# Optimization experiments

Measured on AMD Instinct MI355X. Metric: run time of the kernel, lower is better.

Reference implementation:

```python
import jax, jax.numpy as jnp
import numpy as np

N_NODES = 50_000
N_EDGES = 1_600_000
N_VMS = 10_000
N_SCORE = 1_000_000
D_IN, D_E, D_OUT = 128, 64, 64
MLP_IN, MLP_H, MLP_OUT = 64, 128, 64
H1, H2 = 50, 25  # GNNTower fixed hidden widths


def setup_inputs() -> dict:
    key = jax.random.key(0)
    ks = jax.random.split(key, 24)
    w = lambda k, s: (jax.random.normal(k, s, jnp.float32) * 0.05)
    return {
        "component_features": jax.random.normal(ks[0], (N_NODES, D_IN), jnp.float32),
        "component_edges_features": jax.random.normal(ks[1], (N_EDGES, D_E), jnp.float32),
        "vm_features": jax.random.normal(ks[2], (N_VMS, MLP_IN), jnp.float32),
        "src": jax.random.randint(ks[3], (N_EDGES,), 0, N_NODES, jnp.int32),
        "dst": jax.random.randint(ks[4], (N_EDGES,), 0, N_NODES, jnp.int32),
        "e_comp": jax.random.randint(ks[5], (N_SCORE,), 0, N_NODES, jnp.int32),
        "e_vm": jax.random.randint(ks[6], (N_SCORE,), 0, N_VMS, jnp.int32),
        # GNN layer 1: W_msg [D_IN+D_E, H1], W_apply [D_IN+H1, H1]
        "Wm1": w(ks[7], (D_IN + D_E, H1)), "bm1": jnp.zeros((H1,), jnp.float32),
        "Wa1": w(ks[8], (D_IN + H1, H1)), "ba1": jnp.zeros((H1,), jnp.float32),
        # GNN layer 2
        "Wm2": w(ks[9], (H1 + D_E, H2)), "bm2": jnp.zeros((H2,), jnp.float32),
        "Wa2": w(ks[10], (H1 + H2, H2)), "ba2": jnp.zeros((H2,), jnp.float32),
        # GNN layer 3
        "Wm3": w(ks[11], (H2 + D_E, D_OUT)), "bm3": jnp.zeros((D_OUT,), jnp.float32),
        "Wa3": w(ks[12], (H2 + D_OUT, D_OUT)), "ba3": jnp.zeros((D_OUT,), jnp.float32),
        # MLP tower
        "Wmlp1": w(ks[13], (MLP_IN, MLP_H)), "bmlp1": jnp.zeros((MLP_H,), jnp.float32),
        "Wmlp2": w(ks[14], (MLP_H, MLP_OUT)), "bmlp2": jnp.zeros((MLP_OUT,), jnp.float32),
    }


def reference(component_features, component_edges_features, vm_features,
              src, dst, e_comp, e_vm,
              Wm1, bm1, Wa1, ba1, Wm2, bm2, Wa2, ba2, Wm3, bm3, Wa3, ba3,
              Wmlp1, bmlp1, Wmlp2, bmlp2):
    ef = component_edges_features

    def gnn_layer(h, Wm, bm, Wa, ba):
        d = h.shape[-1]
        # message: relu(W_msg @ concat(h[src], efeat)) == gather + split matmul (avoids concat copy)
        m = jax.nn.relu(h[src] @ Wm[:d] + ef @ Wm[d:] + bm)  # [E, out]
        # scatter-sum aggregation into destination nodes
        h_neigh = jax.ops.segment_sum(m, dst, num_segments=N_NODES)  # [N, out]
        # apply: relu(W_apply @ concat(h, h_neigh))
        return jax.nn.relu(h @ Wa[:d] + h_neigh @ Wa[d:] + ba)

    h = gnn_layer(component_features, Wm1, bm1, Wa1, ba1)   # [N, 50]
    h = gnn_layer(h, Wm2, bm2, Wa2, ba2)                    # [N, 25]  (dropout = identity in eval)
    h = gnn_layer(h, Wm3, bm3, Wa3, ba3)                    # [N, D_OUT]

    vm = jax.nn.relu(vm_features @ Wmlp1 + bmlp1) @ Wmlp2 + bmlp2  # [V, MLP_OUT]

    # sum over concat(comp_emb[e_comp], vm_emb[e_vm]) == sum of parts
    scores = jnp.sum(h, axis=-1)[e_comp] + jnp.sum(vm, axis=-1)[e_vm]  # [N_SCORE]
    return jax.nn.sigmoid(scores)
```

## Files before the change

### kernel.cpp

```cpp
#include <hip/hip_runtime.h>

typedef unsigned int uint;
typedef unsigned short ushort;
typedef short bf16x8 __attribute__((ext_vector_type(8)));
typedef float f32x4  __attribute__((ext_vector_type(4)));


__device__ __forceinline__ ushort f2bf(float f) {
    uint u = __float_as_uint(f);
    u += 0x7FFFu + ((u >> 16) & 1u);
    return (ushort)(u >> 16);
}
__device__ __forceinline__ float bf2f(uint s) {
    return __uint_as_float(s << 16);
}

template<int K0, int KP0, int K1, int KP1, int KC, int OUT, int WOUT,
         int NTC, int RPT, int MODE>
__global__ __launch_bounds__(256) void tile_gemm(
    const float* __restrict__ X0, int sx0,
    const float* __restrict__ X1, int sx1,
    const float* __restrict__ Wg, const float* __restrict__ Bg,
    float* __restrict__ Y, int sy, int nR)
{
    constexpr int KPT  = KP0 + KP1;
    constexpr int C4   = KC / 4;
    constexpr int OUTP = 4 * NTC;
    constexpr int NTR  = 256 / NTC;
    constexpr int TR   = NTR * RPT;
    static_assert(TR == 128, "tile must be 128 rows");
    static_assert(KPT % KC == 0, "KC must divide KPT");

    __shared__ float4 Xl[TR * C4];
    __shared__ float4 Wl[KC * NTC];
    __shared__ float  __align__(16) bl[OUTP];

    const int tid = threadIdx.x;
    const int r0  = blockIdx.x * TR;

    for (int idx = tid; idx < OUTP; idx += 256)
        bl[idx] = (Bg != nullptr && idx < OUT) ? Bg[idx] : 0.f;

    const int tc  = tid & (NTC - 1);
    const int tr  = tid / NTC;
    const int key = (RPT * tr) >> 3;

    float4 acc[RPT];
    #pragma unroll
    for (int i = 0; i < RPT; i++) acc[i] = make_float4(0.f, 0.f, 0.f, 0.f);

    for (int kc0 = 0; kc0 < KPT; kc0 += KC) {
        if (kc0 != 0) __syncthreads();
        for (int idx = tid; idx < TR * C4; idx += 256) {
            int r = idx / C4, c = idx - r * C4;
            int col = kc0 + 4 * c;
            int gr = r0 + r;
            float4 v = make_float4(0.f, 0.f, 0.f, 0.f);
            if (gr < nR) {
                if (KP1 == 0 || col < KP0)
                    v = *reinterpret_cast<const float4*>(X0 + (long long)gr * sx0 + col);
                else
                    v = *reinterpret_cast<const float4*>(X1 + (long long)gr * sx1 + (col - KP0));
            }
            int cs = c + ((r >> 3) % C4); if (cs >= C4) cs -= C4;
            Xl[r * C4 + cs] = v;
        }
        for (int idx = tid; idx < KC * OUTP; idx += 256) {
            int kl = idx / OUTP, o = idx - kl * OUTP;
            int k = kc0 + kl;
            float v = 0.f;
            if (o < OUT) {
                if (k < KP0) { if (k < K0) v = Wg[k * OUT + o]; }
                else { int kk = k - KP0; if (kk < K1) v = Wg[(K0 + kk) * OUT + o]; }
            }
            ((float*)Wl)[kl * OUTP + o] = v;
        }
        __syncthreads();

        const int km = key % C4;
        #pragma unroll 4
        for (int k4 = 0; k4 < C4; k4++) {
            int cs = k4 + km; if (cs >= C4) cs -= C4;
            float4 x[RPT];
            #pragma unroll
            for (int i = 0; i < RPT; i++)
                x[i] = Xl[(RPT * tr + i) * C4 + cs];
            #pragma unroll
            for (int kk = 0; kk < 4; kk++) {
                float4 w = Wl[(4 * k4 + kk) * NTC + tc];
                #pragma unroll
                for (int i = 0; i < RPT; i++) {
                    float xs = (kk == 0) ? x[i].x : (kk == 1) ? x[i].y
                             : (kk == 2) ? x[i].z : x[i].w;
                    acc[i].x = fmaf(xs, w.x, acc[i].x);
                    acc[i].y = fmaf(xs, w.y, acc[i].y);
                    acc[i].z = fmaf(xs, w.z, acc[i].z);
                    acc[i].w = fmaf(xs, w.w, acc[i].w);
                }
            }
        }
    }

    const float4 b4 = reinterpret_cast<float4*>(bl)[tc];
    const int o = 4 * tc;

    if (MODE == 0 || MODE == 1) {
        if (o < WOUT) {
            #pragma unroll
            for (int i = 0; i < RPT; i++) {
                int gr = r0 + RPT * tr + i;
                if (gr < nR) {
                    float4 v;
                    v.x = acc[i].x + b4.x; v.y = acc[i].y + b4.y;
                    v.z = acc[i].z + b4.z; v.w = acc[i].w + b4.w;
                    if (MODE == 1) {
                        v.x = fmaxf(v.x, 0.f); v.y = fmaxf(v.y, 0.f);
                        v.z = fmaxf(v.z, 0.f); v.w = fmaxf(v.w, 0.f);
                    }
                    *reinterpret_cast<float4*>(Y + (long long)gr * sy + o) = v;
                }
            }
        }
    } else {
        #pragma unroll
        for (int i = 0; i < RPT; i++) {
            int gr = r0 + RPT * tr + i;
            float s = fmaxf(acc[i].x + b4.x, 0.f) + fmaxf(acc[i].y + b4.y, 0.f)
                    + fmaxf(acc[i].z + b4.z, 0.f) + fmaxf(acc[i].w + b4.w, 0.f);
            #pragma unroll
            for (int off = 1; off < NTC; off <<= 1) s += __shfl_xor(s, off);
            if (tc == 0 && gr < nR) Y[gr] = s;
        }
    }
}

__global__ __launch_bounds__(256) void proj_all(
    const float* __restrict__ ef,
    const float* __restrict__ W1e, const float* __restrict__ W2e,
    const float* __restrict__ W3e, const int* __restrict__ invperm,
    ushort* __restrict__ G1, ushort* __restrict__ G2, ushort* __restrict__ G3,
    int nE)
{
    constexpr int NT  = 10;
    constexpr int CLP = 168;

    __shared__ ushort Al[64 * 64];
    __shared__ ushort Bl[NT * 128 * 8];
    __shared__ ushort Cl[64 * CLP];
    __shared__ int    sl_pos[64];

    const int tid = threadIdx.x;

    for (int idx = tid; idx < NT * 128; idx += 256) {
        int t  = idx >> 7;
        int ks = (idx >> 6) & 1;
        int l  = idx & 63;
        int gp  = t * 16 + (l & 15);
        int kb  = ks * 32 + ((l >> 4) << 3);
        ushort u[8];
        #pragma unroll
        for (int j = 0; j < 8; j++) {
            int k = kb + j;
            float w = 0.f;
            if (gp < 64)      { if (gp < 50) w = W1e[k * 50 + gp]; }
            else if (gp < 96) { int c = gp - 64; if (c < 25) w = W2e[k * 25 + c]; }
            else              { int c = gp - 96; w = W3e[k * 64 + c]; }
            u[j] = f2bf(w);
        }
        *reinterpret_cast<bf16x8*>(&Bl[idx * 8]) = *reinterpret_cast<bf16x8*>(u);
    }

    const int wv = tid >> 6;
    const int l  = tid & 63;
    const int ntiles = (nE + 63) >> 6;

    for (int tile = blockIdx.x; tile < ntiles; tile += gridDim.x) {
        const int r0 = tile << 6;
        __syncthreads();

        if (tid < 64) sl_pos[tid] = (r0 + tid < nE) ? invperm[r0 + tid] : -1;
        {
            int row = tid >> 2;
            int kq  = (tid & 3) << 4;
            int gr  = r0 + row;
            float4 f0 = {0,0,0,0}, f1 = {0,0,0,0}, f2 = {0,0,0,0}, f3 = {0,0,0,0};
            if (gr < nE) {
                const float* p = ef + (size_t)gr * 64 + kq;
                f0 = *reinterpret_cast<const float4*>(p);
                f1 = *reinterpret_cast<const float4*>(p + 4);
                f2 = *reinterpret_cast<const float4*>(p + 8);
                f3 = *reinterpret_cast<const float4*>(p + 12);
            }
            ushort u[16];
            u[0]=f2bf(f0.x); u[1]=f2bf(f0.y); u[2]=f2bf(f0.z); u[3]=f2bf(f0.w);
            u[4]=f2bf(f1.x); u[5]=f2bf(f1.y); u[6]=f2bf(f1.z); u[7]=f2bf(f1.w);
            u[8]=f2bf(f2.x); u[9]=f2bf(f2.y); u[10]=f2bf(f2.z); u[11]=f2bf(f2.w);
            u[12]=f2bf(f3.x); u[13]=f2bf(f3.y); u[14]=f2bf(f3.z); u[15]=f2bf(f3.w);
            int kc0 = ((kq >> 3) + 0) ^ (row & 7);
            int kc1 = ((kq >> 3) + 1) ^ (row & 7);
            *reinterpret_cast<bf16x8*>(&Al[(row << 6) + kc0 * 8]) = *reinterpret_cast<bf16x8*>(u);
            *reinterpret_cast<bf16x8*>(&Al[(row << 6) + kc1 * 8]) = *reinterpret_cast<bf16x8*>(u + 8);
        }
        __syncthreads();

        f32x4 acc[NT];
        #pragma unroll
        for (int t = 0; t < NT; t++) acc[t] = (f32x4){0.f, 0.f, 0.f, 0.f};
        const int rl = wv * 16 + (l & 15);
        #pragma unroll
        for (int ks = 0; ks < 2; ks++) {
            int kch = (ks * 4 + (l >> 4)) ^ (rl & 7);
            bf16x8 a = *reinterpret_cast<const bf16x8*>(&Al[(rl << 6) + kch * 8]);
            #pragma unroll
            for (int t = 0; t < NT; t++) {
                bf16x8 b = *reinterpret_cast<const bf16x8*>(&Bl[((t * 2 + ks) * 64 + l) * 8]);
                acc[t] = __builtin_amdgcn_mfma_f32_16x16x32_bf16(a, b, acc[t], 0, 0, 0);
            }
        }
        #pragma unroll
        for (int t = 0; t < NT; t++)
            #pragma unroll
            for (int j = 0; j < 4; j++) {
                int rr = wv * 16 + ((l >> 4) << 2) + j;
                Cl[rr * CLP + t * 16 + (l & 15)] = f2bf(acc[t][j]);
            }
        __syncthreads();

        for (int idx = tid; idx < 64 * 20; idx += 256) {
            int row = idx / 20, c = idx - row * 20;
            int pos = sl_pos[row];
            if (pos < 0) continue;
            uint4 v = *reinterpret_cast<const uint4*>(&Cl[row * CLP + c * 8]);
            if (c < 8)
                *reinterpret_cast<uint4*>(G1 + (size_t)pos * 64 + c * 8) = v;
            else if (c < 12)
                *reinterpret_cast<uint4*>(G2 + (size_t)pos * 32 + (c - 8) * 8) = v;
            else
                *reinterpret_cast<uint4*>(G3 + (size_t)pos * 64 + (c - 12) * 8) = v;
        }
    }
}

template<int NT, bool SECB>
__global__ __launch_bounds__(256) void proj_mfma(
    const float* __restrict__ ef,
    const float* __restrict__ WA, int wacols,
    const float* __restrict__ WB, int wbcols,
    const int* __restrict__ invperm,
    ushort* __restrict__ GA, ushort* __restrict__ GB, int nE)
{
    constexpr int NCOL = NT * 16;
    constexpr int CLP  = NCOL + 8;
    constexpr int CPR  = NCOL / 8;
    constexpr int GAS  = SECB ? 64 : NCOL;

    __shared__ ushort Al[64 * 64];
    __shared__ ushort Bl[NT * 128 * 8];
    __shared__ ushort Cl[64 * CLP];
    __shared__ int    sl_pos[64];

    const int tid = threadIdx.x;

    for (int idx = tid; idx < NT * 128; idx += 256) {
        int t  = idx >> 7;
        int ks = (idx >> 6) & 1;
        int l  = idx & 63;
        int col = t * 16 + (l & 15);
        int kb  = ks * 32 + ((l >> 4) << 3);
        ushort u[8];
        #pragma unroll
        for (int j = 0; j < 8; j++) {
            int k = kb + j;
            float w = 0.f;
            if (!SECB || col < 64) { if (col < wacols) w = WA[k * wacols + col]; }
            else { int c2 = col - 64; if (c2 < wbcols) w = WB[k * wbcols + c2]; }
            u[j] = f2bf(w);
        }
        *reinterpret_cast<bf16x8*>(&Bl[idx * 8]) = *reinterpret_cast<bf16x8*>(u);
    }

    const int wv = tid >> 6;
    const int l  = tid & 63;
    const int ntiles = (nE + 63) >> 6;

    for (int tile = blockIdx.x; tile < ntiles; tile += gridDim.x) {
        const int r0 = tile << 6;
        __syncthreads();

        if (tid < 64) sl_pos[tid] = (r0 + tid < nE) ? invperm[r0 + tid] : -1;
        {
            int row = tid >> 2;
            int kq  = (tid & 3) << 4;
            int gr  = r0 + row;
            float4 f0 = {0,0,0,0}, f1 = {0,0,0,0}, f2 = {0,0,0,0}, f3 = {0,0,0,0};
            if (gr < nE) {
                const float* p = ef + (size_t)gr * 64 + kq;
                f0 = *reinterpret_cast<const float4*>(p);
                f1 = *reinterpret_cast<const float4*>(p + 4);
                f2 = *reinterpret_cast<const float4*>(p + 8);
                f3 = *reinterpret_cast<const float4*>(p + 12);
            }
            ushort u[16];
            u[0]=f2bf(f0.x); u[1]=f2bf(f0.y); u[2]=f2bf(f0.z); u[3]=f2bf(f0.w);
            u[4]=f2bf(f1.x); u[5]=f2bf(f1.y); u[6]=f2bf(f1.z); u[7]=f2bf(f1.w);
            u[8]=f2bf(f2.x); u[9]=f2bf(f2.y); u[10]=f2bf(f2.z); u[11]=f2bf(f2.w);
            u[12]=f2bf(f3.x); u[13]=f2bf(f3.y); u[14]=f2bf(f3.z); u[15]=f2bf(f3.w);
            int kc0 = ((kq >> 3) + 0) ^ (row & 7);
            int kc1 = ((kq >> 3) + 1) ^ (row & 7);
            *reinterpret_cast<bf16x8*>(&Al[(row << 6) + kc0 * 8]) = *reinterpret_cast<bf16x8*>(u);
            *reinterpret_cast<bf16x8*>(&Al[(row << 6) + kc1 * 8]) = *reinterpret_cast<bf16x8*>(u + 8);
        }
        __syncthreads();

        f32x4 acc[NT];
        #pragma unroll
        for (int t = 0; t < NT; t++) acc[t] = (f32x4){0.f, 0.f, 0.f, 0.f};
        const int rl = wv * 16 + (l & 15);
        #pragma unroll
        for (int ks = 0; ks < 2; ks++) {
            int kch = (ks * 4 + (l >> 4)) ^ (rl & 7);
            bf16x8 a = *reinterpret_cast<const bf16x8*>(&Al[(rl << 6) + kch * 8]);
            #pragma unroll
            for (int t = 0; t < NT; t++) {
                bf16x8 b = *reinterpret_cast<const bf16x8*>(&Bl[((t * 2 + ks) * 64 + l) * 8]);
                acc[t] = __builtin_amdgcn_mfma_f32_16x16x32_bf16(a, b, acc[t], 0, 0, 0);
            }
        }
        #pragma unroll
        for (int t = 0; t < NT; t++)
            #pragma unroll
            for (int j = 0; j < 4; j++) {
                int rr = wv * 16 + ((l >> 4) << 2) + j;
                Cl[rr * CLP + t * 16 + (l & 15)] = f2bf(acc[t][j]);
            }
        __syncthreads();

        for (int idx = tid; idx < 64 * CPR; idx += 256) {
            int row = idx / CPR, c = idx - row * CPR;
            int pos = sl_pos[row];
            if (pos < 0) continue;
            uint4 v = *reinterpret_cast<const uint4*>(&Cl[row * CLP + c * 8]);
            if (!SECB || c < 8)
                *reinterpret_cast<uint4*>(GA + (size_t)pos * GAS + c * 8) = v;
            else
                *reinterpret_cast<uint4*>(GB + (size_t)pos * 32 + (c - 8) * 8) = v;
        }
    }
}

template<int NCL, int GS, int SP>
__global__ __launch_bounds__(256) void agg_csr(
    const ushort* __restrict__ G, const int* __restrict__ srcp,
    const int* __restrict__ rowp, const float* __restrict__ P,
    float* __restrict__ ng, int nN)
{
    const int o = threadIdx.x & (NCL - 1);
    const int g = threadIdx.x / NCL;
    const int n = blockIdx.x * (256 / NCL) + g;
    if (n >= nN) return;
    const int s0 = rowp[n], s1 = rowp[n + 1];

    float a0=0,a1=0,a2=0,a3=0,a4=0,a5=0,a6=0,a7=0;
    int pos = s0;
    for (; pos + 2 <= s1; pos += 2) {
        int sA = srcp[pos], sB = srcp[pos + 1];
        uint4 gA = *reinterpret_cast<const uint4*>(G + (size_t)pos * GS + o * 8);
        uint4 gB = *reinterpret_cast<const uint4*>(G + (size_t)(pos + 1) * GS + o * 8);
        const float* pA = P + (size_t)sA * SP + o * 8;
        const float* pB = P + (size_t)sB * SP + o * 8;
        float4 pa0 = *reinterpret_cast<const float4*>(pA);
        float4 pa1 = *reinterpret_cast<const float4*>(pA + 4);
        float4 pb0 = *reinterpret_cast<const float4*>(pB);
        float4 pb1 = *reinterpret_cast<const float4*>(pB + 4);
        a0 += fmaxf(pa0.x + bf2f(gA.x & 0xffffu), 0.f) + fmaxf(pb0.x + bf2f(gB.x & 0xffffu), 0.f);
        a1 += fmaxf(pa0.y + bf2f(gA.x >> 16), 0.f)     + fmaxf(pb0.y + bf2f(gB.x >> 16), 0.f);
        a2 += fmaxf(pa0.z + bf2f(gA.y & 0xffffu), 0.f) + fmaxf(pb0.z + bf2f(gB.y & 0xffffu), 0.f);
        a3 += fmaxf(pa0.w + bf2f(gA.y >> 16), 0.f)     + fmaxf(pb0.w + bf2f(gB.y >> 16), 0.f);
        a4 += fmaxf(pa1.x + bf2f(gA.z & 0xffffu), 0.f) + fmaxf(pb1.x + bf2f(gB.z & 0xffffu), 0.f);
        a5 += fmaxf(pa1.y + bf2f(gA.z >> 16), 0.f)     + fmaxf(pb1.y + bf2f(gB.z >> 16), 0.f);
        a6 += fmaxf(pa1.z + bf2f(gA.w & 0xffffu), 0.f) + fmaxf(pb1.z + bf2f(gB.w & 0xffffu), 0.f);
        a7 += fmaxf(pa1.w + bf2f(gA.w >> 16), 0.f)     + fmaxf(pb1.w + bf2f(gB.w >> 16), 0.f);
    }
    if (pos < s1) {
        int sA = srcp[pos];
        uint4 gA = *reinterpret_cast<const uint4*>(G + (size_t)pos * GS + o * 8);
        const float* pA = P + (size_t)sA * SP + o * 8;
        float4 pa0 = *reinterpret_cast<const float4*>(pA);
        float4 pa1 = *reinterpret_cast<const float4*>(pA + 4);
        a0 += fmaxf(pa0.x + bf2f(gA.x & 0xffffu), 0.f);
        a1 += fmaxf(pa0.y + bf2f(gA.x >> 16), 0.f);
        a2 += fmaxf(pa0.z + bf2f(gA.y & 0xffffu), 0.f);
        a3 += fmaxf(pa0.w + bf2f(gA.y >> 16), 0.f);
        a4 += fmaxf(pa1.x + bf2f(gA.z & 0xffffu), 0.f);
        a5 += fmaxf(pa1.y + bf2f(gA.z >> 16), 0.f);
        a6 += fmaxf(pa1.z + bf2f(gA.w & 0xffffu), 0.f);
        a7 += fmaxf(pa1.w + bf2f(gA.w >> 16), 0.f);
    }
    float4 w0 = {a0, a1, a2, a3}, w1 = {a4, a5, a6, a7};
    float* yp = ng + (size_t)n * 64 + o * 8;
    *reinterpret_cast<float4*>(yp)     = w0;
    *reinterpret_cast<float4*>(yp + 4) = w1;
}

__global__ __launch_bounds__(256) void hist_kernel(
    const int* __restrict__ dst, int* __restrict__ deg, int nE)
{
    for (int e = blockIdx.x * 256 + threadIdx.x; e < nE; e += gridDim.x * 256)
        atomicAdd(&deg[dst[e]], 1);
}

__global__ __launch_bounds__(256) void scan_blksum(
    const int* __restrict__ deg, int* __restrict__ bsum, int nN)
{
    const int t = threadIdx.x;
    const int base = blockIdx.x * 1024;
    int s = 0;
    for (int i = t; i < 1024; i += 256) {
        int id = base + i;
        s += (id < nN) ? deg[id] : 0;
    }
    #pragma unroll
    for (int off = 32; off > 0; off >>= 1) s += __shfl_down(s, off);
    __shared__ int w[4];
    if ((t & 63) == 0) w[t >> 6] = s;
    __syncthreads();
    if (t == 0) bsum[blockIdx.x] = w[0] + w[1] + w[2] + w[3];
}

__global__ __launch_bounds__(256) void scan_top(
    int* __restrict__ bsum, int nB, int* __restrict__ rowp, int nN)
{
    const int t = threadIdx.x;
    int v = (t < nB) ? bsum[t] : 0;
    int x = v;
    #pragma unroll
    for (int off = 1; off < 64; off <<= 1) {
        int u = __shfl_up(x, off);
        if ((t & 63) >= off) x += u;
    }
    __shared__ int wsum[4];
    if ((t & 63) == 63) wsum[t >> 6] = x;
    __syncthreads();
    int add = 0;
    #pragma unroll
    for (int i = 0; i < 4; i++) if (i < (t >> 6)) add += wsum[i];
    x += add;
    if (t < nB) bsum[t] = x - v;
    if (t == nB - 1) rowp[nN] = x;
}

__global__ __launch_bounds__(256) void scan_final(
    const int* __restrict__ deg, const int* __restrict__ bsum,
    int* __restrict__ rowp, int nN)
{
    const int t = threadIdx.x;
    const int idx0 = blockIdx.x * 1024 + t * 4;
    int e[4];
    #pragma unroll
    for (int i = 0; i < 4; i++) {
        int id = idx0 + i;
        e[i] = (id < nN) ? deg[id] : 0;
    }
    int tl = e[0] + e[1] + e[2] + e[3];
    int x = tl;
    #pragma unroll
    for (int off = 1; off < 64; off <<= 1) {
        int u = __shfl_up(x, off);
        if ((t & 63) >= off) x += u;
    }
    __shared__ int wsum[4];
    if ((t & 63) == 63) wsum[t >> 6] = x;
    __syncthreads();
    int add = 0;
    #pragma unroll
    for (int i = 0; i < 4; i++) if (i < (t >> 6)) add += wsum[i];
    int run = (x - tl) + add + bsum[blockIdx.x];
    #pragma unroll
    for (int i = 0; i < 4; i++) {
        int id = idx0 + i;
        if (id < nN) rowp[id] = run;
        run += e[i];
    }
}

__global__ __launch_bounds__(256) void scatter_kernel(
    const int* __restrict__ src, const int* __restrict__ dst,
    const int* __restrict__ rowp, int* __restrict__ cursor,
    int* __restrict__ srcp, int* __restrict__ invperm, int nE)
{
    for (int e = blockIdx.x * 256 + threadIdx.x; e < nE; e += gridDim.x * 256) {
        int d = dst[e];
        int pos = rowp[d] + atomicAdd(&cursor[d], 1);
        srcp[pos] = src[e];
        invperm[e] = pos;
    }
}

__global__ void w2sum_kernel(const float* __restrict__ W2, const float* __restrict__ b2,
                             float* __restrict__ w2s)
{
    int j = threadIdx.x;
    float s = 0.f;
    for (int o = 0; o < 64; o++) s += W2[j * 64 + o];
    w2s[j] = s;
    if (j == 0) {
        float bs = 0.f;
        for (int o = 0; o < 64; o++) bs += b2[o];
        w2s[128] = bs;
    }
}

__global__ __launch_bounds__(256) void vm_kernel(
    const float* __restrict__ vmf, const float* __restrict__ W1,
    const float* __restrict__ b1, const float* __restrict__ w2s,
    float* __restrict__ vm_sum, int nV)
{
    const int lane = threadIdx.x & 63;
    const int grp  = threadIdx.x >> 6;
    for (int v = blockIdx.x * 4 + grp; v < nV; v += gridDim.x * 4) {
        const float* vr = vmf + (long long)v * 64;
        float a0 = b1[lane], a1 = b1[lane + 64];
        #pragma unroll 4
        for (int k = 0; k < 64; k += 4) {
            float4 x = *reinterpret_cast<const float4*>(vr + k);
            a0 = fmaf(x.x, W1[(k + 0) * 128 + lane], a0);
            a0 = fmaf(x.y, W1[(k + 1) * 128 + lane], a0);
            a0 = fmaf(x.z, W1[(k + 2) * 128 + lane], a0);
            a0 = fmaf(x.w, W1[(k + 3) * 128 + lane], a0);
            a1 = fmaf(x.x, W1[(k + 0) * 128 + lane + 64], a1);
            a1 = fmaf(x.y, W1[(k + 1) * 128 + lane + 64], a1);
            a1 = fmaf(x.z, W1[(k + 2) * 128 + lane + 64], a1);
            a1 = fmaf(x.w, W1[(k + 3) * 128 + lane + 64], a1);
        }
        float part = fmaxf(a0, 0.f) * w2s[lane] + fmaxf(a1, 0.f) * w2s[lane + 64];
        #pragma unroll
        for (int off = 32; off > 0; off >>= 1) part += __shfl_down(part, off);
        if (lane == 0) vm_sum[v] = part + w2s[128];
    }
}

__global__ __launch_bounds__(256) void score_kernel(
    const int* __restrict__ ec, const int* __restrict__ ev,
    const float* __restrict__ ns, const float* __restrict__ vs,
    float* __restrict__ out, int n)
{
    int i = blockIdx.x * blockDim.x + threadIdx.x;
    if (i < n) {
        float x = ns[ec[i]] + vs[ev[i]];
        out[i] = 1.f / (1.f + expf(-x));
    }
}

extern "C" void kernel_launch(void* const* d_in, const int* in_sizes, int n_in,
                              void* d_out, int out_size, void* d_ws, size_t ws_size,
                              hipStream_t stream)
{
    const float* comp = (const float*)d_in[0];
    const float* ef   = (const float*)d_in[1];
    const float* vmf  = (const float*)d_in[2];
    const int*   src  = (const int*)d_in[3];
    const int*   dst  = (const int*)d_in[4];
    const int*   ecmp = (const int*)d_in[5];
    const int*   evm  = (const int*)d_in[6];
    const float* Wm1 = (const float*)d_in[7];  const float* bm1 = (const float*)d_in[8];
    const float* Wa1 = (const float*)d_in[9];  const float* ba1 = (const float*)d_in[10];
    const float* Wm2 = (const float*)d_in[11]; const float* bm2 = (const float*)d_in[12];
    const float* Wa2 = (const float*)d_in[13]; const float* ba2 = (const float*)d_in[14];
    const float* Wm3 = (const float*)d_in[15]; const float* bm3 = (const float*)d_in[16];
    const float* Wa3 = (const float*)d_in[17]; const float* ba3 = (const float*)d_in[18];
    const float* W1  = (const float*)d_in[19]; const float* b1  = (const float*)d_in[20];
    const float* W2  = (const float*)d_in[21]; const float* b2  = (const float*)d_in[22];

    const int nN = in_sizes[0] / 128;
    const int nE = in_sizes[3];
    const int nV = in_sizes[2] / 64;
    const int nS = in_sizes[5];

    float* ws = (float*)d_ws;
    float* bufA     = ws;
    float* bufB     = bufA + (size_t)nN * 64;
    float* ng       = bufB + (size_t)nN * 64;
    float* node_sum = ng + (size_t)nN * 64;
    float* vm_sum   = node_sum + nN;
    float* w2s      = vm_sum + nV;
    int*   iws      = (int*)(w2s + 132);
    int*   deg      = iws;
    int*   cursor   = deg + nN;
    int*   rowp     = cursor + nN;
    int*   srcp     = rowp + nN + 1;
    int*   invperm  = srcp + nE;
    int*   bsum     = invperm + nE;
    size_t Goff = (((size_t)((char*)(bsum + 256) - (char*)d_ws)) + 255) & ~(size_t)255;
    ushort* G1 = (ushort*)((char*)d_ws + Goff);
    const size_t need_single = (size_t)nE * (64 + 32 + 64) * 2;
    const bool single  = (Goff + need_single) <= ws_size;
    const bool twopass = !single && (Goff + (size_t)nE * 96 * 2) <= ws_size;
    ushort* G2 = single ? (G1 + (size_t)nE * 64)
               : twopass ? (G1 + (size_t)nE * 64) : G1;
    ushort* G3 = single ? (G2 + (size_t)nE * 32) : G1;

    float* h1 = bufA;
    float* h2 = bufB;
    float* P1 = bufB;
    float* P2 = bufB;
    float* P3 = bufA;

    const float* We1 = Wm1 + 128 * 50;
    const float* We2 = Wm2 + 50 * 25;
    const float* We3 = Wm3 + 25 * 64;

    const int ngrid  = (nN + 127) / 128;
    const int ptiles = (nE + 63) / 64;
    const int pgrid  = ptiles < 2048 ? ptiles : 2048;
    const int a8grid = (nN * 8 + 255) / 256;
    const int a4grid = (nN * 4 + 255) / 256;
    const int sgrid  = (nE + 255) / 256 < 4096 ? (nE + 255) / 256 : 4096;
    const int nB     = (nN + 1023) / 1024;

    hipMemsetAsync(deg, 0, (size_t)(2 * nN) * sizeof(int), stream);
    hist_kernel<<<sgrid, 256, 0, stream>>>(dst, deg, nE);
    scan_blksum<<<nB, 256, 0, stream>>>(deg, bsum, nN);
    scan_top<<<1, 256, 0, stream>>>(bsum, nB, rowp, nN);
    scan_final<<<nB, 256, 0, stream>>>(deg, bsum, rowp, nN);
    scatter_kernel<<<sgrid, 256, 0, stream>>>(src, dst, rowp, cursor, srcp, invperm, nE);

    if (single) {
        proj_all<<<pgrid, 256, 0, stream>>>(ef, We1, We2, We3, invperm, G1, G2, G3, nE);
    } else if (twopass) {
        proj_mfma<6, true><<<pgrid, 256, 0, stream>>>(ef, We1, 50, We2, 25, invperm, G1, G2, nE);
    } else {
        proj_mfma<4, false><<<pgrid, 256, 0, stream>>>(ef, We1, 50, nullptr, 0, invperm, G1, nullptr, nE);
    }

    tile_gemm<128,128, 0,0, 64, 50, 64, 16, 8, 0><<<ngrid, 256, 0, stream>>>(
        comp, 128, nullptr, 0, Wm1, bm1, P1, 64, nN);
    agg_csr<8, 64, 64><<<a8grid, 256, 0, stream>>>(G1, srcp, rowp, P1, ng, nN);
    if (!single && !twopass)
        proj_mfma<2, false><<<pgrid, 256, 0, stream>>>(ef, We2, 25, nullptr, 0, invperm, G2, nullptr, nE);
    tile_gemm<128,128, 50,52, 60, 50, 52, 16, 8, 1><<<ngrid, 256, 0, stream>>>(
        comp, 128, ng, 64, Wa1, ba1, h1, 52, nN);
    if (!single && twopass)
        proj_mfma<4, false><<<pgrid, 256, 0, stream>>>(ef, We3, 64, nullptr, 0, invperm, G1, nullptr, nE);

    tile_gemm<50,52, 0,0, 52, 25, 32, 8, 4, 0><<<ngrid, 256, 0, stream>>>(
        h1, 52, nullptr, 0, Wm2, bm2, P2, 32, nN);
    agg_csr<4, 32, 32><<<a4grid, 256, 0, stream>>>(G2, srcp, rowp, P2, ng, nN);
    if (!single && !twopass)
        proj_mfma<4, false><<<pgrid, 256, 0, stream>>>(ef, We3, 64, nullptr, 0, invperm, G1, nullptr, nE);
    tile_gemm<50,52, 25,28, 80, 25, 28, 8, 4, 1><<<ngrid, 256, 0, stream>>>(
        h1, 52, ng, 64, Wa2, ba2, h2, 28, nN);

    tile_gemm<25,28, 0,0, 28, 64, 64, 16, 8, 0><<<ngrid, 256, 0, stream>>>(
        h2, 28, nullptr, 0, Wm3, bm3, P3, 64, nN);
    agg_csr<8, 64, 64><<<a8grid, 256, 0, stream>>>(G3, srcp, rowp, P3, ng, nN);
    tile_gemm<25,28, 64,68, 48, 64, 64, 16, 8, 2><<<ngrid, 256, 0, stream>>>(
        h2, 28, ng, 64, Wa3, ba3, node_sum, 1, nN);

    w2sum_kernel<<<1, 128, 0, stream>>>(W2, b2, w2s);
    vm_kernel<<<(nV + 3) / 4, 256, 0, stream>>>(vmf, W1, b1, w2s, vm_sum, nV);
    score_kernel<<<(nS + 255) / 256, 256, 0, stream>>>(ecmp, evm, node_sum, vm_sum, (float*)d_out, nS);
}
```

Measured before the change: 802.6 us.

## Gather edge features in CSR order and write projections in 4-edge interleaved layout

The projection kernels now read edge features through a forward permutation (CSR position to original edge) and write bf16 MFMA results directly from registers in a layout that groups 4 consecutive CSR edges per column. This drops the LDS staging, the extra barrier and the scattered invperm stores. The aggregation kernel reads these grouped rows with wide loads and picks out the per-edge values. Other changes: node GEMM tiles shrink to 64 rows for more blocks, the w2sum kernel is folded into vm_kernel, and the two-pass fallback is removed. The cost is that the edge-feature reads become random gathers instead of sequential streaming.

```diff
diff --git a/kernel.cpp b/kernel.cpp
--- a/kernel.cpp
+++ b/kernel.cpp
@@ -11,8 +11,10 @@
     u += 0x7FFFu + ((u >> 16) & 1u);
     return (ushort)(u >> 16);
 }
-__device__ __forceinline__ float bf2f(uint s) {
-    return __uint_as_float(s << 16);
+__device__ __forceinline__ uint cvtpk(float lo, float hi) {
+    uint r;
+    asm("v_cvt_pk_bf16_f32 %0, %1, %2" : "=v"(r) : "v"(lo), "v"(hi));
+    return r;
 }
 
 template<int K0, int KP0, int K1, int KP1, int KC, int OUT, int WOUT,
@@ -28,7 +30,7 @@
     constexpr int OUTP = 4 * NTC;
     constexpr int NTR  = 256 / NTC;
     constexpr int TR   = NTR * RPT;
-    static_assert(TR == 128, "tile must be 128 rows");
+    static_assert(TR == 64 || TR == 128, "tile rows");
     static_assert(KPT % KC == 0, "KC must divide KPT");
 
     __shared__ float4 Xl[TR * C4];
@@ -134,20 +136,40 @@
     }
 }
 
-__global__ __launch_bounds__(256) void proj_all(
+__device__ __forceinline__ void proj_stage_A(
+    ushort* Al, const float* __restrict__ ef, const int* __restrict__ perm,
+    int r0, int nE, int tid)
+{
+    int row = tid >> 2;
+    int kq  = (tid & 3) << 4;
+    int gr  = r0 + row;
+    long long e = (gr < nE) ? (long long)perm[gr] : 0;
+    const float* p = ef + e * 64 + kq;
+    float4 f0 = *reinterpret_cast<const float4*>(p);
+    float4 f1 = *reinterpret_cast<const float4*>(p + 4);
+    float4 f2 = *reinterpret_cast<const float4*>(p + 8);
+    float4 f3 = *reinterpret_cast<const float4*>(p + 12);
+    ushort u[16];
+    u[0]=f2bf(f0.x); u[1]=f2bf(f0.y); u[2]=f2bf(f0.z); u[3]=f2bf(f0.w);
+    u[4]=f2bf(f1.x); u[5]=f2bf(f1.y); u[6]=f2bf(f1.z); u[7]=f2bf(f1.w);
+    u[8]=f2bf(f2.x); u[9]=f2bf(f2.y); u[10]=f2bf(f2.z); u[11]=f2bf(f2.w);
+    u[12]=f2bf(f3.x); u[13]=f2bf(f3.y); u[14]=f2bf(f3.z); u[15]=f2bf(f3.w);
+    int kc0 = ((kq >> 3) + 0) ^ (row & 7);
+    int kc1 = ((kq >> 3) + 1) ^ (row & 7);
+    *reinterpret_cast<bf16x8*>(&Al[(row << 6) + kc0 * 8]) = *reinterpret_cast<bf16x8*>(u);
+    *reinterpret_cast<bf16x8*>(&Al[(row << 6) + kc1 * 8]) = *reinterpret_cast<bf16x8*>(u + 8);
+}
+
+__global__ __launch_bounds__(256) void proj_fused(
     const float* __restrict__ ef,
     const float* __restrict__ W1e, const float* __restrict__ W2e,
-    const float* __restrict__ W3e, const int* __restrict__ invperm,
+    const float* __restrict__ W3e, const int* __restrict__ perm,
     ushort* __restrict__ G1, ushort* __restrict__ G2, ushort* __restrict__ G3,
     int nE)
 {
-    constexpr int NT  = 10;
-    constexpr int CLP = 168;
-
+    constexpr int NT = 10;
     __shared__ ushort Al[64 * 64];
     __shared__ ushort Bl[NT * 128 * 8];
-    __shared__ ushort Cl[64 * CLP];
-    __shared__ int    sl_pos[64];
 
     const int tid = threadIdx.x;
 
@@ -177,30 +199,7 @@
     for (int tile = blockIdx.x; tile < ntiles; tile += gridDim.x) {
         const int r0 = tile << 6;
         __syncthreads();
-
-        if (tid < 64) sl_pos[tid] = (r0 + tid < nE) ? invperm[r0 + tid] : -1;
-        {
-            int row = tid >> 2;
-            int kq  = (tid & 3) << 4;
-            int gr  = r0 + row;
-            float4 f0 = {0,0,0,0}, f1 = {0,0,0,0}, f2 = {0,0,0,0}, f3 = {0,0,0,0};
-            if (gr < nE) {
-                const float* p = ef + (size_t)gr * 64 + kq;
-                f0 = *reinterpret_cast<const float4*>(p);
-                f1 = *reinterpret_cast<const float4*>(p + 4);
-                f2 = *reinterpret_cast<const float4*>(p + 8);
-                f3 = *reinterpret_cast<const float4*>(p + 12);
-            }
-            ushort u[16];
-            u[0]=f2bf(f0.x); u[1]=f2bf(f0.y); u[2]=f2bf(f0.z); u[3]=f2bf(f0.w);
-            u[4]=f2bf(f1.x); u[5]=f2bf(f1.y); u[6]=f2bf(f1.z); u[7]=f2bf(f1.w);
-            u[8]=f2bf(f2.x); u[9]=f2bf(f2.y); u[10]=f2bf(f2.z); u[11]=f2bf(f2.w);
-            u[12]=f2bf(f3.x); u[13]=f2bf(f3.y); u[14]=f2bf(f3.z); u[15]=f2bf(f3.w);
-            int kc0 = ((kq >> 3) + 0) ^ (row & 7);
-            int kc1 = ((kq >> 3) + 1) ^ (row & 7);
-            *reinterpret_cast<bf16x8*>(&Al[(row << 6) + kc0 * 8]) = *reinterpret_cast<bf16x8*>(u);
-            *reinterpret_cast<bf16x8*>(&Al[(row << 6) + kc1 * 8]) = *reinterpret_cast<bf16x8*>(u + 8);
-        }
+        proj_stage_A(Al, ef, perm, r0, nE, tid);
         __syncthreads();
 
         f32x4 acc[NT];
@@ -217,47 +216,34 @@
                 acc[t] = __builtin_amdgcn_mfma_f32_16x16x32_bf16(a, b, acc[t], 0, 0, 0);
             }
         }
-        #pragma unroll
-        for (int t = 0; t < NT; t++)
-            #pragma unroll
-            for (int j = 0; j < 4; j++) {
-                int rr = wv * 16 + ((l >> 4) << 2) + j;
-                Cl[rr * CLP + t * 16 + (l & 15)] = f2bf(acc[t][j]);
-            }
-        __syncthreads();
-
-        for (int idx = tid; idx < 64 * 20; idx += 256) {
-            int row = idx / 20, c = idx - row * 20;
-            int pos = sl_pos[row];
-            if (pos < 0) continue;
-            uint4 v = *reinterpret_cast<const uint4*>(&Cl[row * CLP + c * 8]);
-            if (c < 8)
-                *reinterpret_cast<uint4*>(G1 + (size_t)pos * 64 + c * 8) = v;
-            else if (c < 12)
-                *reinterpret_cast<uint4*>(G2 + (size_t)pos * 32 + (c - 8) * 8) = v;
-            else
-                *reinterpret_cast<uint4*>(G3 + (size_t)pos * 64 + (c - 12) * 8) = v;
-        }
-    }
-}
-
-template<int NT, bool SECB>
-__global__ __launch_bounds__(256) void proj_mfma(
+
+        const int grpS = (r0 >> 2) + (wv << 2) + (l >> 4);
+        const int pos0 = grpS << 2;
+        const bool v01 = (pos0 < nE);
+        const bool v23 = (pos0 + 2 < nE);
+        const int c = l & 15;
+        #pragma unroll
+        for (int t = 0; t < NT; t++) {
+            uint p01 = cvtpk(acc[t][0], acc[t][1]);
+            uint p23 = cvtpk(acc[t][2], acc[t][3]);
+            ushort* Gp; size_t idx;
+            if (t < 4)      { Gp = G1; idx = (size_t)grpS * 256 + (t * 16 + c) * 4; }
+            else if (t < 6) { Gp = G2; idx = (size_t)grpS * 128 + ((t - 4) * 16 + c) * 4; }
+            else            { Gp = G3; idx = (size_t)grpS * 256 + ((t - 6) * 16 + c) * 4; }
+            if (v01) *reinterpret_cast<uint*>(Gp + idx)     = p01;
+            if (v23) *reinterpret_cast<uint*>(Gp + idx + 2) = p23;
+        }
+    }
+}
+
+template<int NT, int GS>
+__global__ __launch_bounds__(256) void proj_single(
     const float* __restrict__ ef,
-    const float* __restrict__ WA, int wacols,
-    const float* __restrict__ WB, int wbcols,
-    const int* __restrict__ invperm,
-    ushort* __restrict__ GA, ushort* __restrict__ GB, int nE)
-{
-    constexpr int NCOL = NT * 16;
-    constexpr int CLP  = NCOL + 8;
-    constexpr int CPR  = NCOL / 8;
-    constexpr int GAS  = SECB ? 64 : NCOL;
-
+    const float* __restrict__ W, int wcols,
+    const int* __restrict__ perm, ushort* __restrict__ G, int nE)
+{
     __shared__ ushort Al[64 * 64];
     __shared__ ushort Bl[NT * 128 * 8];
-    __shared__ ushort Cl[64 * CLP];
-    __shared__ int    sl_pos[64];
 
     const int tid = threadIdx.x;
 
@@ -271,9 +257,7 @@
         #pragma unroll
         for (int j = 0; j < 8; j++) {
             int k = kb + j;
-            float w = 0.f;
-            if (!SECB || col < 64) { if (col < wacols) w = WA[k * wacols + col]; }
-            else { int c2 = col - 64; if (c2 < wbcols) w = WB[k * wbcols + c2]; }
+            float w = (col < wcols) ? W[k * wcols + col] : 0.f;
             u[j] = f2bf(w);
         }
         *reinterpret_cast<bf16x8*>(&Bl[idx * 8]) = *reinterpret_cast<bf16x8*>(u);
@@ -286,30 +270,7 @@
     for (int tile = blockIdx.x; tile < ntiles; tile += gridDim.x) {
         const int r0 = tile << 6;
         __syncthreads();
-
-        if (tid < 64) sl_pos[tid] = (r0 + tid < nE) ? invperm[r0 + tid] : -1;
-        {
-            int row = tid >> 2;
-            int kq  = (tid & 3) << 4;
-            int gr  = r0 + row;
-            float4 f0 = {0,0,0,0}, f1 = {0,0,0,0}, f2 = {0,0,0,0}, f3 = {0,0,0,0};
-            if (gr < nE) {
-                const float* p = ef + (size_t)gr * 64 + kq;
-                f0 = *reinterpret_cast<const float4*>(p);
-                f1 = *reinterpret_cast<const float4*>(p + 4);
-                f2 = *reinterpret_cast<const float4*>(p + 8);
-                f3 = *reinterpret_cast<const float4*>(p + 12);
-            }
-            ushort u[16];
-            u[0]=f2bf(f0.x); u[1]=f2bf(f0.y); u[2]=f2bf(f0.z); u[3]=f2bf(f0.w);
-            u[4]=f2bf(f1.x); u[5]=f2bf(f1.y); u[6]=f2bf(f1.z); u[7]=f2bf(f1.w);
-            u[8]=f2bf(f2.x); u[9]=f2bf(f2.y); u[10]=f2bf(f2.z); u[11]=f2bf(f2.w);
-            u[12]=f2bf(f3.x); u[13]=f2bf(f3.y); u[14]=f2bf(f3.z); u[15]=f2bf(f3.w);
-            int kc0 = ((kq >> 3) + 0) ^ (row & 7);
-            int kc1 = ((kq >> 3) + 1) ^ (row & 7);
-            *reinterpret_cast<bf16x8*>(&Al[(row << 6) + kc0 * 8]) = *reinterpret_cast<bf16x8*>(u);
-            *reinterpret_cast<bf16x8*>(&Al[(row << 6) + kc1 * 8]) = *reinterpret_cast<bf16x8*>(u + 8);
-        }
+        proj_stage_A(Al, ef, perm, r0, nE, tid);
         __syncthreads();
 
         f32x4 acc[NT];
@@ -326,24 +287,19 @@
                 acc[t] = __builtin_amdgcn_mfma_f32_16x16x32_bf16(a, b, acc[t], 0, 0, 0);
             }
         }
-        #pragma unroll
-        for (int t = 0; t < NT; t++)
-            #pragma unroll
-            for (int j = 0; j < 4; j++) {
-                int rr = wv * 16 + ((l >> 4) << 2) + j;
-                Cl[rr * CLP + t * 16 + (l & 15)] = f2bf(acc[t][j]);
-            }
-        __syncthreads();
-
-        for (int idx = tid; idx < 64 * CPR; idx += 256) {
-            int row = idx / CPR, c = idx - row * CPR;
-            int pos = sl_pos[row];
-            if (pos < 0) continue;
-            uint4 v = *reinterpret_cast<const uint4*>(&Cl[row * CLP + c * 8]);
-            if (!SECB || c < 8)
-                *reinterpret_cast<uint4*>(GA + (size_t)pos * GAS + c * 8) = v;
-            else
-                *reinterpret_cast<uint4*>(GB + (size_t)pos * 32 + (c - 8) * 8) = v;
+
+        const int grpS = (r0 >> 2) + (wv << 2) + (l >> 4);
+        const int pos0 = grpS << 2;
+        const bool v01 = (pos0 < nE);
+        const bool v23 = (pos0 + 2 < nE);
+        const int c = l & 15;
+        #pragma unroll
+        for (int t = 0; t < NT; t++) {
+            uint p01 = cvtpk(acc[t][0], acc[t][1]);
+            uint p23 = cvtpk(acc[t][2], acc[t][3]);
+            size_t idx = (size_t)grpS * (GS * 4) + (t * 16 + c) * 4;
+            if (v01) *reinterpret_cast<uint*>(G + idx)     = p01;
+            if (v23) *reinterpret_cast<uint*>(G + idx + 2) = p23;
         }
     }
 }
@@ -360,43 +316,41 @@
     if (n >= nN) return;
     const int s0 = rowp[n], s1 = rowp[n + 1];
 
-    float a0=0,a1=0,a2=0,a3=0,a4=0,a5=0,a6=0,a7=0;
-    int pos = s0;
-    for (; pos + 2 <= s1; pos += 2) {
-        int sA = srcp[pos], sB = srcp[pos + 1];
-        uint4 gA = *reinterpret_cast<const uint4*>(G + (size_t)pos * GS + o * 8);
-        uint4 gB = *reinterpret_cast<const uint4*>(G + (size_t)(pos + 1) * GS + o * 8);
-        const float* pA = P + (size_t)sA * SP + o * 8;
-        const float* pB = P + (size_t)sB * SP + o * 8;
-        float4 pa0 = *reinterpret_cast<const float4*>(pA);
-        float4 pa1 = *reinterpret_cast<const float4*>(pA + 4);
-        float4 pb0 = *reinterpret_cast<const float4*>(pB);
-        float4 pb1 = *reinterpret_cast<const float4*>(pB + 4);
-        a0 += fmaxf(pa0.x + bf2f(gA.x & 0xffffu), 0.f) + fmaxf(pb0.x + bf2f(gB.x & 0xffffu), 0.f);
-        a1 += fmaxf(pa0.y + bf2f(gA.x >> 16), 0.f)     + fmaxf(pb0.y + bf2f(gB.x >> 16), 0.f);
-        a2 += fmaxf(pa0.z + bf2f(gA.y & 0xffffu), 0.f) + fmaxf(pb0.z + bf2f(gB.y & 0xffffu), 0.f);
-        a3 += fmaxf(pa0.w + bf2f(gA.y >> 16), 0.f)     + fmaxf(pb0.w + bf2f(gB.y >> 16), 0.f);
-        a4 += fmaxf(pa1.x + bf2f(gA.z & 0xffffu), 0.f) + fmaxf(pb1.x + bf2f(gB.z & 0xffffu), 0.f);
-        a5 += fmaxf(pa1.y + bf2f(gA.z >> 16), 0.f)     + fmaxf(pb1.y + bf2f(gB.z >> 16), 0.f);
-        a6 += fmaxf(pa1.z + bf2f(gA.w & 0xffffu), 0.f) + fmaxf(pb1.z + bf2f(gB.w & 0xffffu), 0.f);
-        a7 += fmaxf(pa1.w + bf2f(gA.w >> 16), 0.f)     + fmaxf(pb1.w + bf2f(gB.w >> 16), 0.f);
-    }
-    if (pos < s1) {
-        int sA = srcp[pos];
-        uint4 gA = *reinterpret_cast<const uint4*>(G + (size_t)pos * GS + o * 8);
-        const float* pA = P + (size_t)sA * SP + o * 8;
-        float4 pa0 = *reinterpret_cast<const float4*>(pA);
-        float4 pa1 = *reinterpret_cast<const float4*>(pA + 4);
-        a0 += fmaxf(pa0.x + bf2f(gA.x & 0xffffu), 0.f);
-        a1 += fmaxf(pa0.y + bf2f(gA.x >> 16), 0.f);
-        a2 += fmaxf(pa0.z + bf2f(gA.y & 0xffffu), 0.f);
-        a3 += fmaxf(pa0.w + bf2f(gA.y >> 16), 0.f);
-        a4 += fmaxf(pa1.x + bf2f(gA.z & 0xffffu), 0.f);
-        a5 += fmaxf(pa1.y + bf2f(gA.z >> 16), 0.f);
-        a6 += fmaxf(pa1.z + bf2f(gA.w & 0xffffu), 0.f);
-        a7 += fmaxf(pa1.w + bf2f(gA.w >> 16), 0.f);
-    }
-    float4 w0 = {a0, a1, a2, a3}, w1 = {a4, a5, a6, a7};
+    float a[8];
+    #pragma unroll
+    for (int j = 0; j < 8; j++) a[j] = 0.f;
+
+    if (s0 < s1) {
+        const int g0 = s0 >> 2, g1 = (s1 - 1) >> 2;
+        for (int grp = g0; grp <= g1; grp++) {
+            uint4 c4[4];
+            const ushort* gb = G + (size_t)grp * (GS * 4) + o * 32;
+            c4[0] = *reinterpret_cast<const uint4*>(gb);
+            c4[1] = *reinterpret_cast<const uint4*>(gb + 8);
+            c4[2] = *reinterpret_cast<const uint4*>(gb + 16);
+            c4[3] = *reinterpret_cast<const uint4*>(gb + 24);
+            const uint* cu = reinterpret_cast<const uint*>(c4);
+            int4 s4 = *reinterpret_cast<const int4*>(srcp + grp * 4);
+            const int* sp = reinterpret_cast<const int*>(&s4);
+            int rlo = s0 - grp * 4; if (rlo < 0) rlo = 0;
+            int rhi = s1 - grp * 4; if (rhi > 4) rhi = 4;
+            for (int r = rlo; r < rhi; r++) {
+                const float* pp = P + (size_t)sp[r] * SP + o * 8;
+                float4 pa = *reinterpret_cast<const float4*>(pp);
+                float4 pb = *reinterpret_cast<const float4*>(pp + 4);
+                float pv[8] = {pa.x, pa.y, pa.z, pa.w, pb.x, pb.y, pb.z, pb.w};
+                #pragma unroll
+                for (int k = 0; k < 8; k++) {
+                    uint lo = cu[(k >> 1) * 4 + (k & 1) * 2 + 0];
+                    uint hi = cu[(k >> 1) * 4 + (k & 1) * 2 + 1];
+                    uint q = (r & 2) ? hi : lo;
+                    uint v = (r & 1) ? (q & 0xffff0000u) : (q << 16);
+                    a[k] += fmaxf(pv[k] + __uint_as_float(v), 0.f);
+                }
+            }
+        }
+    }
+    float4 w0 = {a[0], a[1], a[2], a[3]}, w1 = {a[4], a[5], a[6], a[7]};
     float* yp = ng + (size_t)n * 64 + o * 8;
     *reinterpret_cast<float4*>(yp)     = w0;
     *reinterpret_cast<float4*>(yp + 4) = w1;
@@ -486,37 +440,36 @@
 __global__ __launch_bounds__(256) void scatter_kernel(
     const int* __restrict__ src, const int* __restrict__ dst,
     const int* __restrict__ rowp, int* __restrict__ cursor,
-    int* __restrict__ srcp, int* __restrict__ invperm, int nE)
+    int* __restrict__ srcp, int* __restrict__ perm, int nE)
 {
     for (int e = blockIdx.x * 256 + threadIdx.x; e < nE; e += gridDim.x * 256) {
         int d = dst[e];
         int pos = rowp[d] + atomicAdd(&cursor[d], 1);
         srcp[pos] = src[e];
-        invperm[e] = pos;
-    }
-}
-
-__global__ void w2sum_kernel(const float* __restrict__ W2, const float* __restrict__ b2,
-                             float* __restrict__ w2s)
-{
-    int j = threadIdx.x;
-    float s = 0.f;
-    for (int o = 0; o < 64; o++) s += W2[j * 64 + o];
-    w2s[j] = s;
-    if (j == 0) {
+        perm[pos] = e;
+    }
+}
+
+__global__ __launch_bounds__(256) void vm_kernel(
+    const float* __restrict__ vmf, const float* __restrict__ W1,
+    const float* __restrict__ b1, const float* __restrict__ W2,
+    const float* __restrict__ b2, float* __restrict__ vm_sum, int nV)
+{
+    __shared__ float w2s[132];
+    const int tid = threadIdx.x;
+    if (tid < 128) {
+        float s = 0.f;
+        for (int o = 0; o < 64; o++) s += W2[tid * 64 + o];
+        w2s[tid] = s;
+    } else if (tid == 128) {
         float bs = 0.f;
         for (int o = 0; o < 64; o++) bs += b2[o];
         w2s[128] = bs;
     }
-}
-
-__global__ __launch_bounds__(256) void vm_kernel(
-    const float* __restrict__ vmf, const float* __restrict__ W1,
-    const float* __restrict__ b1, const float* __restrict__ w2s,
-    float* __restrict__ vm_sum, int nV)
-{
-    const int lane = threadIdx.x & 63;
-    const int grp  = threadIdx.x >> 6;
+    __syncthreads();
+
+    const int lane = tid & 63;
+    const int grp  = tid >> 6;
     for (int v = blockIdx.x * 4 + grp; v < nV; v += gridDim.x * 4) {
         const float* vr = vmf + (long long)v * 64;
         float a0 = b1[lane], a1 = b1[lane + 64];
@@ -575,6 +528,7 @@
     const int nE = in_sizes[3];
     const int nV = in_sizes[2] / 64;
     const int nS = in_sizes[5];
+    const int nE4 = (nE + 63) & ~63;
 
     float* ws = (float*)d_ws;
     float* bufA     = ws;
@@ -582,22 +536,19 @@
     float* ng       = bufB + (size_t)nN * 64;
     float* node_sum = ng + (size_t)nN * 64;
     float* vm_sum   = node_sum + nN;
-    float* w2s      = vm_sum + nV;
-    int*   iws      = (int*)(w2s + 132);
+    int*   iws      = (int*)(((size_t)(vm_sum + nV) + 15) & ~(size_t)15);
     int*   deg      = iws;
     int*   cursor   = deg + nN;
     int*   rowp     = cursor + nN;
-    int*   srcp     = rowp + nN + 1;
-    int*   invperm  = srcp + nE;
-    int*   bsum     = invperm + nE;
-    size_t Goff = (((size_t)((char*)(bsum + 256) - (char*)d_ws)) + 255) & ~(size_t)255;
+    int*   bsum     = rowp + nN + 1;
+    int*   srcp     = (int*)(((size_t)(bsum + 256) + 15) & ~(size_t)15);
+    int*   perm     = srcp + nE;
+    size_t Goff = (((size_t)((char*)(perm + nE) - (char*)d_ws)) + 255) & ~(size_t)255;
     ushort* G1 = (ushort*)((char*)d_ws + Goff);
-    const size_t need_single = (size_t)nE * (64 + 32 + 64) * 2;
-    const bool single  = (Goff + need_single) <= ws_size;
-    const bool twopass = !single && (Goff + (size_t)nE * 96 * 2) <= ws_size;
-    ushort* G2 = single ? (G1 + (size_t)nE * 64)
-               : twopass ? (G1 + (size_t)nE * 64) : G1;
-    ushort* G3 = single ? (G2 + (size_t)nE * 32) : G1;
+    const size_t g1u = (size_t)nE4 * 64, g2u = (size_t)nE4 * 32, g3u = (size_t)nE4 * 64;
+    const bool single = (Goff + (g1u + g2u + g3u) * 2) <= ws_size;
+    ushort* G2 = single ? (G1 + g1u) : G1;
+    ushort* G3 = single ? (G2 + g2u) : G1;
 
     float* h1 = bufA;
     float* h2 = bufB;
@@ -609,8 +560,8 @@
     const float* We2 = Wm2 + 50 * 25;
     const float* We3 = Wm3 + 25 * 64;
 
-    const int ngrid  = (nN + 127) / 128;
-    const int ptiles = (nE + 63) / 64;
+    const int ngrid  = (nN + 63) / 64;
+    const int ptiles = nE4 / 64;
     const int pgrid  = ptiles < 2048 ? ptiles : 2048;
     const int a8grid = (nN * 8 + 255) / 256;
     const int a4grid = (nN * 4 + 255) / 256;
@@ -622,41 +573,35 @@
     scan_blksum<<<nB, 256, 0, stream>>>(deg, bsum, nN);
     scan_top<<<1, 256, 0, stream>>>(bsum, nB, rowp, nN);
     scan_final<<<nB, 256, 0, stream>>>(deg, bsum, rowp, nN);
-    scatter_kernel<<<sgrid, 256, 0, stream>>>(src, dst, rowp, cursor, srcp, invperm, nE);
-
-    if (single) {
-        proj_all<<<pgrid, 256, 0, stream>>>(ef, We1, We2, We3, invperm, G1, G2, G3, nE);
-    } else if (twopass) {
-        proj_mfma<6, true><<<pgrid, 256, 0, stream>>>(ef, We1, 50, We2, 25, invperm, G1, G2, nE);
-    } else {
-        proj_mfma<4, false><<<pgrid, 256, 0, stream>>>(ef, We1, 50, nullptr, 0, invperm, G1, nullptr, nE);
-    }
-
-    tile_gemm<128,128, 0,0, 64, 50, 64, 16, 8, 0><<<ngrid, 256, 0, stream>>>(
+    scatter_kernel<<<sgrid, 256, 0, stream>>>(src, dst, rowp, cursor, srcp, perm, nE);
+
+    if (single)
+        proj_fused<<<pgrid, 256, 0, stream>>>(ef, We1, We2, We3, perm, G1, G2, G3, nE);
+    else
+        proj_single<4, 64><<<pgrid, 256, 0, stream>>>(ef, We1, 50, perm, G1, nE);
+
+    tile_gemm<128,128, 0,0, 64, 50, 64, 16, 4, 0><<<ngrid, 256, 0, stream>>>(
         comp, 128, nullptr, 0, Wm1, bm1, P1, 64, nN);
     agg_csr<8, 64, 64><<<a8grid, 256, 0, stream>>>(G1, srcp, rowp, P1, ng, nN);
-    if (!single && !twopass)
-        proj_mfma<2, false><<<pgrid, 256, 0, stream>>>(ef, We2, 25, nullptr, 0, invperm, G2, nullptr, nE);
-    tile_gemm<128,128, 50,52, 60, 50, 52, 16, 8, 1><<<ngrid, 256, 0, stream>>>(
+    if (!single)
+        proj_single<2, 32><<<pgrid, 256, 0, stream>>>(ef, We2, 25, perm, G2, nE);
+    tile_gemm<128,128, 50,52, 60, 50, 52, 16, 4, 1><<<ngrid, 256, 0, stream>>>(
         comp, 128, ng, 64, Wa1, ba1, h1, 52, nN);
-    if (!single && twopass)
-        proj_mfma<4, false><<<pgrid, 256, 0, stream>>>(ef, We3, 64, nullptr, 0, invperm, G1, nullptr, nE);
-
-    tile_gemm<50,52, 0,0, 52, 25, 32, 8, 4, 0><<<ngrid, 256, 0, stream>>>(
+
+    tile_gemm<50,52, 0,0, 52, 25, 32, 8, 2, 0><<<ngrid, 256, 0, stream>>>(
         h1, 52, nullptr, 0, Wm2, bm2, P2, 32, nN);
     agg_csr<4, 32, 32><<<a4grid, 256, 0, stream>>>(G2, srcp, rowp, P2, ng, nN);
-    if (!single && !twopass)
-        proj_mfma<4, false><<<pgrid, 256, 0, stream>>>(ef, We3, 64, nullptr, 0, invperm, G1, nullptr, nE);
-    tile_gemm<50,52, 25,28, 80, 25, 28, 8, 4, 1><<<ngrid, 256, 0, stream>>>(
+    if (!single)
+        proj_single<4, 64><<<pgrid, 256, 0, stream>>>(ef, We3, 64, perm, G3, nE);
+    tile_gemm<50,52, 25,28, 80, 25, 28, 8, 2, 1><<<ngrid, 256, 0, stream>>>(
         h1, 52, ng, 64, Wa2, ba2, h2, 28, nN);
 
-    tile_gemm<25,28, 0,0, 28, 64, 64, 16, 8, 0><<<ngrid, 256, 0, stream>>>(
+    tile_gemm<25,28, 0,0, 28, 64, 64, 16, 4, 0><<<ngrid, 256, 0, stream>>>(
         h2, 28, nullptr, 0, Wm3, bm3, P3, 64, nN);
     agg_csr<8, 64, 64><<<a8grid, 256, 0, stream>>>(G3, srcp, rowp, P3, ng, nN);
-    tile_gemm<25,28, 64,68, 48, 64, 64, 16, 8, 2><<<ngrid, 256, 0, stream>>>(
+    tile_gemm<25,28, 64,68, 48, 64, 64, 16, 4, 2><<<ngrid, 256, 0, stream>>>(
         h2, 28, ng, 64, Wa3, ba3, node_sum, 1, nN);
 
-    w2sum_kernel<<<1, 128, 0, stream>>>(W2, b2, w2s);
-    vm_kernel<<<(nV + 3) / 4, 256, 0, stream>>>(vmf, W1, b1, w2s, vm_sum, nV);
+    vm_kernel<<<(nV + 3) / 4, 256, 0, stream>>>(vmf, W1, b1, W2, b2, vm_sum, nV);
     score_kernel<<<(nS + 255) / 256, 256, 0, stream>>>(ecmp, evm, node_sum, vm_sum, (float*)d_out, nS);
 }
```

After: 848.7 us. 5.7% more time.
